# Kernel optimization log

Measured on AMD Instinct MI355X. Metric: run time of the kernel, lower is better.

The kernel has to match this reference:

```python
import jax, jax.numpy as jnp
import numpy as np

N = 100000   # nodes
E = 1600000  # edges
IN, HID, OUT = 128, 128, 64  # hidden = 2 * out_channels per GCNEncoder


def setup_inputs() -> dict:
    key = jax.random.key(0)
    k = jax.random.split(key, 5)
    x = jax.random.normal(k[0], (N, IN), dtype=jnp.float32)
    edge_index = jax.random.randint(k[1], (2, E), 0, N, dtype=jnp.int32)
    # Glorot-style init like PyG GCNConv
    W1 = jax.random.normal(k[2], (IN, HID), dtype=jnp.float32) * (1.0 / np.sqrt(IN))
    b1 = jnp.zeros((HID,), dtype=jnp.float32)
    W2 = jax.random.normal(k[3], (HID, OUT), dtype=jnp.float32) * (1.0 / np.sqrt(HID))
    b2 = jnp.zeros((OUT,), dtype=jnp.float32)
    return {"x": x, "edge_index": edge_index, "W1": W1, "b1": b1, "W2": W2, "b2": b2}


def gcn_conv(x, row, col, W, b):
    # x: [N, F_in]; row/col: [E+N] (edge_index with self-loops appended)
    h = x @ W                                      # dense transform [N, F_out]
    deg = jax.ops.segment_sum(jnp.ones_like(col, dtype=h.dtype), col, num_segments=N)
    dinv = jnp.where(deg > 0, jax.lax.rsqrt(deg), 0.0)
    norm = dinv[row] * dinv[col]                   # symmetric normalization per edge
    msg = h[row] * norm[:, None]                   # gather + scale: [E+N, F_out]
    out = jax.ops.segment_sum(msg, col, num_segments=N)  # scatter-add to targets
    return out + b


def reference(x, edge_index, W1, b1, W2, b2):
    loops = jnp.arange(N, dtype=edge_index.dtype)
    row = jnp.concatenate([edge_index[0], loops])  # sources
    col = jnp.concatenate([edge_index[1], loops])  # targets
    h = jax.nn.relu(gcn_conv(x, row, col, W1, b1))
    return gcn_conv(h, row, col, W2, b2)
```

## Files before the change

### kernel.cpp

```cpp
#include <hip/hip_runtime.h>
#include <hip/hip_fp16.h>

#define N_NODES 100000
#define N_EDGES 1600000
#define K_DIM   128

#define CHUNK_LG 8
#define CHUNK    256
#define NBKT     ((N_NODES + CHUNK - 1) / CHUNK)
#define CAP      4608
#define EPB      1024
#define NBLK_A   ((N_EDGES + EPB - 1) / EPB)
#define G1_BLOCKS ((N_NODES + 63) / 64)

typedef _Float16 half8 __attribute__((ext_vector_type(8)));
typedef float    f32x4 __attribute__((ext_vector_type(4)));

__global__ __launch_bounds__(256) void k_gemm1_bucket(
    const float* __restrict__ x, const float* __restrict__ W,
    _Float16* __restrict__ Hout,
    const int* __restrict__ row, const int* __restrict__ col,
    int* __restrict__ gcur, int* __restrict__ pairs)
{
    __shared__ __align__(16) char smem[128 * 136 * 2];

    if (blockIdx.x & 1) {
        constexpr int KD = K_DIM, NOUT = 128, NT = NOUT / 16;
        _Float16 (*Blds)[KD + 8] = reinterpret_cast<_Float16(*)[KD + 8]>(smem);

        for (int i = threadIdx.x * 4; i < KD * NOUT; i += 256 * 4) {
            int k = i / NOUT, n = i % NOUT;
            float4 wv = *reinterpret_cast<const float4*>(W + i);
            Blds[n + 0][k] = (_Float16)wv.x;
            Blds[n + 1][k] = (_Float16)wv.y;
            Blds[n + 2][k] = (_Float16)wv.z;
            Blds[n + 3][k] = (_Float16)wv.w;
        }
        __syncthreads();

        const int tile = blockIdx.x >> 1;
        const int wave = threadIdx.x >> 6;
        const int lane = threadIdx.x & 63;
        const int r16  = lane & 15;
        const int kg   = lane >> 4;
        const int arow = tile * 64 + wave * 16 + r16;
        const bool rowok = arow < N_NODES;

        f32x4 acc[NT];
#pragma unroll
        for (int ct = 0; ct < NT; ++ct) acc[ct] = (f32x4){0.f, 0.f, 0.f, 0.f};

#pragma unroll
        for (int kc = 0; kc < KD / 32; ++kc) {
            const int k0 = kc * 32 + kg * 8;
            float4 xa = make_float4(0.f, 0.f, 0.f, 0.f), xb = xa;
            if (rowok) {
                const float4* ap = reinterpret_cast<const float4*>(
                    x + (size_t)arow * KD + k0);
                xa = ap[0]; xb = ap[1];
            }
            half8 a;
            a[0] = (_Float16)xa.x; a[1] = (_Float16)xa.y;
            a[2] = (_Float16)xa.z; a[3] = (_Float16)xa.w;
            a[4] = (_Float16)xb.x; a[5] = (_Float16)xb.y;
            a[6] = (_Float16)xb.z; a[7] = (_Float16)xb.w;
#pragma unroll
            for (int ct = 0; ct < NT; ++ct) {
                half8 b = *reinterpret_cast<const half8*>(&Blds[ct * 16 + r16][k0]);
                acc[ct] = __builtin_amdgcn_mfma_f32_16x16x32_f16(a, b, acc[ct], 0, 0, 0);
            }
        }

        const int orow0 = tile * 64 + wave * 16 + kg * 4;
#pragma unroll
        for (int r = 0; r < 4; ++r) {
            int orow = orow0 + r;
            if (orow < N_NODES) {
#pragma unroll
                for (int ct = 0; ct < NT; ++ct)
                    Hout[(size_t)orow * NOUT + ct * 16 + r16] = (_Float16)acc[ct][r];
            }
        }
    } else {
        int* hist  = (int*)smem;
        int* sbase = hist + 512;
        int* lcur  = hist + 1024;
        int t = threadIdx.x;
        for (int i = t; i < NBKT; i += 256) { hist[i] = 0; lcur[i] = 0; }
        __syncthreads();
        int base = (blockIdx.x >> 1) * EPB;
        int myb[4], myp[4];
#pragma unroll
        for (int j = 0; j < 4; ++j) {
            int i = base + t + j * 256;
            int b = -1, p = 0;
            if (i < N_EDGES) {
                int r = row[i], c = col[i];
                b = c >> CHUNK_LG;
                p = ((c & (CHUNK - 1)) << 17) | r;
                atomicAdd(&hist[b], 1);
            }
            myb[j] = b; myp[j] = p;
        }
        __syncthreads();
        for (int i = t; i < NBKT; i += 256) {
            int c = hist[i];
            sbase[i] = c ? atomicAdd(&gcur[i], c) : 0;
        }
        __syncthreads();
#pragma unroll
        for (int j = 0; j < 4; ++j) {
            int b = myb[j];
            if (b >= 0) {
                int pos = sbase[b] + atomicAdd(&lcur[b], 1);
                pairs[b * CAP + pos] = myp[j];
            }
        }
    }
}

__global__ __launch_bounds__(256) void k_fillB(const int* __restrict__ gcur,
                                               const int* __restrict__ pairs,
                                               int* __restrict__ rowptr,
                                               float* __restrict__ dinv,
                                               int* __restrict__ srows) {
    __shared__ int red[256];
    __shared__ int psum[256];
    __shared__ int deg[CHUNK];
    __shared__ int curs[CHUNK];
    int b = blockIdx.x, t = threadIdx.x;

    int part = 0;
    for (int i = t; i < NBKT; i += 256)
        if (i < b) part += gcur[i];
    red[t] = part;
    __syncthreads();
    for (int off = 128; off; off >>= 1) {
        if (t < off) red[t] += red[t + off];
        __syncthreads();
    }
    int gb = red[0];
    int cnt = gcur[b];
    if (b == 0 && t == 0) rowptr[N_NODES] = N_EDGES;

    int nbase = b << CHUNK_LG;
    const int* mp = pairs + b * CAP;

    deg[t] = 0;
    __syncthreads();
    for (int i = t; i < cnt; i += 256) atomicAdd(&deg[mp[i] >> 17], 1);
    __syncthreads();

    int d = deg[t];
    psum[t] = d;
    __syncthreads();
    for (int off = 1; off < 256; off <<= 1) {
        int u = (t >= off) ? psum[t - off] : 0;
        __syncthreads();
        psum[t] += u;
        __syncthreads();
    }
    int o = gb + psum[t] - d;
    curs[t] = o;
    int node = nbase + t;
    if (node < N_NODES) {
        rowptr[node] = o;
        dinv[node] = rsqrtf(1.f + (float)d);
    }
    __syncthreads();
    for (int i = t; i < cnt; i += 256) {
        int v = mp[i];
        int pos = atomicAdd(&curs[v >> 17], 1);
        srows[pos] = v & 0x1FFFF;
    }
}

template<int NOUT>
__global__ __launch_bounds__(256) void k_gemm_mfma2(
    const _Float16* __restrict__ Ah, const float* __restrict__ W,
    const float* __restrict__ b_in, _Float16* __restrict__ Hout, int nrows)
{
    constexpr int KD = K_DIM;
    constexpr int NT = NOUT / 16;
    __shared__ _Float16 Blds[NOUT][KD + 8];

    for (int i = threadIdx.x * 4; i < KD * NOUT; i += 256 * 4) {
        int k = i / NOUT, n = i % NOUT;
        float4 wv = *reinterpret_cast<const float4*>(W + i);
        Blds[n + 0][k] = (_Float16)wv.x;
        Blds[n + 1][k] = (_Float16)wv.y;
        Blds[n + 2][k] = (_Float16)wv.z;
        Blds[n + 3][k] = (_Float16)wv.w;
    }
    __syncthreads();

    const int wave = threadIdx.x >> 6;
    const int lane = threadIdx.x & 63;
    const int r16  = lane & 15;
    const int kg   = lane >> 4;
    const int arow = blockIdx.x * 64 + wave * 16 + r16;
    const bool rowok = arow < nrows;

    f32x4 acc[NT];
#pragma unroll
    for (int ct = 0; ct < NT; ++ct) acc[ct] = (f32x4){0.f, 0.f, 0.f, 0.f};

#pragma unroll
    for (int kc = 0; kc < KD / 32; ++kc) {
        const int k0 = kc * 32 + kg * 8;
        uint4 raw = make_uint4(0, 0, 0, 0);
        if (rowok)
            raw = *reinterpret_cast<const uint4*>(Ah + (size_t)arow * KD + k0);
        union { uint4 u; _Float16 h[8]; } U; U.u = raw;
        float4 bA = *reinterpret_cast<const float4*>(b_in + k0);
        float4 bB = *reinterpret_cast<const float4*>(b_in + k0 + 4);
        half8 a;
        a[0] = (_Float16)fmaxf((float)U.h[0] + bA.x, 0.f);
        a[1] = (_Float16)fmaxf((float)U.h[1] + bA.y, 0.f);
        a[2] = (_Float16)fmaxf((float)U.h[2] + bA.z, 0.f);
        a[3] = (_Float16)fmaxf((float)U.h[3] + bA.w, 0.f);
        a[4] = (_Float16)fmaxf((float)U.h[4] + bB.x, 0.f);
        a[5] = (_Float16)fmaxf((float)U.h[5] + bB.y, 0.f);
        a[6] = (_Float16)fmaxf((float)U.h[6] + bB.z, 0.f);
        a[7] = (_Float16)fmaxf((float)U.h[7] + bB.w, 0.f);
#pragma unroll
        for (int ct = 0; ct < NT; ++ct) {
            half8 b = *reinterpret_cast<const half8*>(&Blds[ct * 16 + r16][k0]);
            acc[ct] = __builtin_amdgcn_mfma_f32_16x16x32_f16(a, b, acc[ct], 0, 0, 0);
        }
    }

    const int orow0 = blockIdx.x * 64 + wave * 16 + kg * 4;
#pragma unroll
    for (int r = 0; r < 4; ++r) {
        int orow = orow0 + r;
        if (orow < nrows) {
#pragma unroll
            for (int ct = 0; ct < NT; ++ct)
                Hout[(size_t)orow * NOUT + ct * 16 + r16] = (_Float16)acc[ct][r];
        }
    }
}

__device__ __forceinline__ void fma8(uint4 v, float wgt, float (&acc)[8]) {
    union { uint4 u; _Float16 h[8]; } U;
    U.u = v;
#pragma unroll
    for (int j = 0; j < 8; ++j)
        acc[j] = fmaf((float)U.h[j], wgt, acc[j]);
}

template<int F, bool OUT_HALF>
__global__ __launch_bounds__(256) void k_gather_h(
    const int* __restrict__ rowptr, const int* __restrict__ srows,
    const float* __restrict__ dinv, const _Float16* __restrict__ H,
    const float* __restrict__ bias, void* __restrict__ OUT, int n)
{
    constexpr int LPR = F / 8;
    constexpr int GR  = 64 / LPR;
    int w = blockIdx.x * 4 + (threadIdx.x >> 6);
    if (w >= n) return;
    int lane = threadIdx.x & 63;
    int g = lane / LPR;
    int c = lane % LPR;
    float di = dinv[w];
    int s = rowptr[w], e = rowptr[w + 1];
    const uint4* Hp = reinterpret_cast<const uint4*>(H);

    float acc[8];
#pragma unroll
    for (int j = 0; j < 8; ++j) acc[j] = 0.f;
    uint4 hv = Hp[(size_t)w * LPR + c];
    fma8(hv, (g == 0) ? di * di : 0.f, acc);

    if (s < e) {
        int k0 = s + g;
        int kc = min(k0, e - 1);
        int r  = srows[kc];
        float wcur = (k0 < e) ? dinv[r] * di : 0.f;
        uint4 hcur = Hp[(size_t)r * LPR + c];
        for (int k = s + GR; k < e; k += GR) {
            int k1  = k + g;
            int kc1 = min(k1, e - 1);
            int r1  = srows[kc1];
            float wnxt = (k1 < e) ? dinv[r1] * di : 0.f;
            uint4 hnxt = Hp[(size_t)r1 * LPR + c];
            fma8(hcur, wcur, acc);
            wcur = wnxt; hcur = hnxt;
        }
        fma8(hcur, wcur, acc);
    }

#pragma unroll
    for (int m = 32; m >= LPR; m >>= 1) {
#pragma unroll
        for (int j = 0; j < 8; ++j)
            acc[j] += __shfl_xor(acc[j], m, 64);
    }

    if (g == 0) {
        if constexpr (OUT_HALF) {
            union { uint4 u; __half2 h[4]; } P;
#pragma unroll
            for (int j = 0; j < 4; ++j)
                P.h[j] = __floats2half2_rn(acc[2 * j], acc[2 * j + 1]);
            reinterpret_cast<uint4*>(OUT)[(size_t)w * LPR + c] = P.u;
        } else {
            const float4* bp = reinterpret_cast<const float4*>(bias + c * 8);
            float4 b0 = bp[0], b1 = bp[1];
            float4 o0 = make_float4(acc[0] + b0.x, acc[1] + b0.y,
                                    acc[2] + b0.z, acc[3] + b0.w);
            float4 o1 = make_float4(acc[4] + b1.x, acc[5] + b1.y,
                                    acc[6] + b1.z, acc[7] + b1.w);
            float* op = (float*)OUT + (size_t)w * F + c * 8;
            *reinterpret_cast<float4*>(op)     = o0;
            *reinterpret_cast<float4*>(op + 4) = o1;
        }
    }
}


extern "C" void kernel_launch(void* const* d_in, const int* in_sizes, int n_in,
                              void* d_out, int out_size, void* d_ws, size_t ws_size,
                              hipStream_t stream) {
    const float* x  = (const float*)d_in[0];
    const int*   ei = (const int*)  d_in[1];
    const float* W1 = (const float*)d_in[2];
    const float* b1 = (const float*)d_in[3];
    const float* W2 = (const float*)d_in[4];
    const float* b2 = (const float*)d_in[5];
    float* out = (float*)d_out;

    const int* row = ei;
    const int* col = ei + N_EDGES;

    char* ws = (char*)d_ws;
    int*   gcur   = (int*)ws;
    int*   rowptr = gcur + 512;
    float* dinv   = (float*)(rowptr + ((N_NODES + 256) & ~255));
    int*   srows  = (int*)(dinv + ((N_NODES + 255) & ~255));
    _Float16* bufH   = (_Float16*)(srows + ((N_EDGES + 255) & ~255));
    _Float16* bufAgg = bufH + (size_t)N_NODES * 128;
    int*   pairs  = (int*)bufAgg;

    hipMemsetAsync(gcur, 0, NBKT * sizeof(int), stream);
    k_gemm1_bucket<<<G1_BLOCKS + NBLK_A, 256, 0, stream>>>(
        x, W1, bufH, row, col, gcur, pairs);

    k_fillB<<<NBKT, 256, 0, stream>>>(gcur, pairs, rowptr, dinv, srows);

    k_gather_h<128, true><<<(N_NODES + 3) / 4, 256, 0, stream>>>(
        rowptr, srows, dinv, bufH, nullptr, bufAgg, N_NODES);

    k_gemm_mfma2<64><<<(N_NODES + 63) / 64, 256, 0, stream>>>(
        bufAgg, W2, b1, bufH, N_NODES);

    k_gather_h<64, false><<<(N_NODES + 3) / 4, 256, 0, stream>>>(
        rowptr, srows, dinv, bufH, b2, out, N_NODES);
}
```

Baseline: 216.5 us.

## Fuse first-layer aggregation with second GEMM and rebalance bucket blocks

Replaces the separate layer-1 gather kernel and the second MFMA GEMM with one kernel. Each block aggregates 32 nodes into shared memory, applies bias and ReLU, and multiplies by W2 with MFMA, so the aggregated 128-wide fp16 matrix is never written to or read back from global memory. The edge-bucketing part now handles 4096 edges per block, with bucket blocks interleaved one in five among the GEMM blocks. The CSR fill kernel stages each bucket's pairs in shared memory so they are read from global memory once instead of twice. In exchange, every fused block converts W2 into shared memory again, and the fused kernel's occupancy and register pressure differ from the split kernels.

After: 204.9 us. 1.06x faster.

```diff
diff --git a/kernel.cpp b/kernel.cpp
--- a/kernel.cpp
+++ b/kernel.cpp
@@ -9,9 +9,10 @@
 #define CHUNK    256
 #define NBKT     ((N_NODES + CHUNK - 1) / CHUNK)
 #define CAP      4608
-#define EPB      1024
+#define EPB      4096
 #define NBLK_A   ((N_EDGES + EPB - 1) / EPB)
 #define G1_BLOCKS ((N_NODES + 63) / 64)
+#define NBLK_TOT (G1_BLOCKS + NBLK_A)
 
 typedef _Float16 half8 __attribute__((ext_vector_type(8)));
 typedef float    f32x4 __attribute__((ext_vector_type(4)));
@@ -24,7 +25,7 @@
 {
     __shared__ __align__(16) char smem[128 * 136 * 2];
 
-    if (blockIdx.x & 1) {
+    if (blockIdx.x % 5 != 0) {
         constexpr int KD = K_DIM, NOUT = 128, NT = NOUT / 16;
         _Float16 (*Blds)[KD + 8] = reinterpret_cast<_Float16(*)[KD + 8]>(smem);
 
@@ -38,7 +39,7 @@
         }
         __syncthreads();
 
-        const int tile = blockIdx.x >> 1;
+        const int tile = blockIdx.x - blockIdx.x / 5 - 1;
         const int wave = threadIdx.x >> 6;
         const int lane = threadIdx.x & 63;
         const int r16  = lane & 15;
@@ -88,10 +89,10 @@
         int t = threadIdx.x;
         for (int i = t; i < NBKT; i += 256) { hist[i] = 0; lcur[i] = 0; }
         __syncthreads();
-        int base = (blockIdx.x >> 1) * EPB;
-        int myb[4], myp[4];
-#pragma unroll
-        for (int j = 0; j < 4; ++j) {
+        int base = (blockIdx.x / 5) * EPB;
+        int myb[16], myp[16];
+#pragma unroll
+        for (int j = 0; j < 16; ++j) {
             int i = base + t + j * 256;
             int b = -1, p = 0;
             if (i < N_EDGES) {
@@ -109,7 +110,7 @@
         }
         __syncthreads();
 #pragma unroll
-        for (int j = 0; j < 4; ++j) {
+        for (int j = 0; j < 16; ++j) {
             int b = myb[j];
             if (b >= 0) {
                 int pos = sbase[b] + atomicAdd(&lcur[b], 1);
@@ -124,6 +125,7 @@
                                                int* __restrict__ rowptr,
                                                float* __restrict__ dinv,
                                                int* __restrict__ srows) {
+    __shared__ int mpl[CAP];
     __shared__ int red[256];
     __shared__ int psum[256];
     __shared__ int deg[CHUNK];
@@ -134,6 +136,7 @@
     for (int i = t; i < NBKT; i += 256)
         if (i < b) part += gcur[i];
     red[t] = part;
+    deg[t] = 0;
     __syncthreads();
     for (int off = 128; off; off >>= 1) {
         if (t < off) red[t] += red[t + off];
@@ -146,9 +149,11 @@
     int nbase = b << CHUNK_LG;
     const int* mp = pairs + b * CAP;
 
-    deg[t] = 0;
-    __syncthreads();
-    for (int i = t; i < cnt; i += 256) atomicAdd(&deg[mp[i] >> 17], 1);
+    for (int i = t; i < cnt; i += 256) {
+        int v = mp[i];
+        mpl[i] = v;
+        atomicAdd(&deg[v >> 17], 1);
+    }
     __syncthreads();
 
     int d = deg[t];
@@ -169,76 +174,9 @@
     }
     __syncthreads();
     for (int i = t; i < cnt; i += 256) {
-        int v = mp[i];
+        int v = mpl[i];
         int pos = atomicAdd(&curs[v >> 17], 1);
         srows[pos] = v & 0x1FFFF;
-    }
-}
-
-template<int NOUT>
-__global__ __launch_bounds__(256) void k_gemm_mfma2(
-    const _Float16* __restrict__ Ah, const float* __restrict__ W,
-    const float* __restrict__ b_in, _Float16* __restrict__ Hout, int nrows)
-{
-    constexpr int KD = K_DIM;
-    constexpr int NT = NOUT / 16;
-    __shared__ _Float16 Blds[NOUT][KD + 8];
-
-    for (int i = threadIdx.x * 4; i < KD * NOUT; i += 256 * 4) {
-        int k = i / NOUT, n = i % NOUT;
-        float4 wv = *reinterpret_cast<const float4*>(W + i);
-        Blds[n + 0][k] = (_Float16)wv.x;
-        Blds[n + 1][k] = (_Float16)wv.y;
-        Blds[n + 2][k] = (_Float16)wv.z;
-        Blds[n + 3][k] = (_Float16)wv.w;
-    }
-    __syncthreads();
-
-    const int wave = threadIdx.x >> 6;
-    const int lane = threadIdx.x & 63;
-    const int r16  = lane & 15;
-    const int kg   = lane >> 4;
-    const int arow = blockIdx.x * 64 + wave * 16 + r16;
-    const bool rowok = arow < nrows;
-
-    f32x4 acc[NT];
-#pragma unroll
-    for (int ct = 0; ct < NT; ++ct) acc[ct] = (f32x4){0.f, 0.f, 0.f, 0.f};
-
-#pragma unroll
-    for (int kc = 0; kc < KD / 32; ++kc) {
-        const int k0 = kc * 32 + kg * 8;
-        uint4 raw = make_uint4(0, 0, 0, 0);
-        if (rowok)
-            raw = *reinterpret_cast<const uint4*>(Ah + (size_t)arow * KD + k0);
-        union { uint4 u; _Float16 h[8]; } U; U.u = raw;
-        float4 bA = *reinterpret_cast<const float4*>(b_in + k0);
-        float4 bB = *reinterpret_cast<const float4*>(b_in + k0 + 4);
-        half8 a;
-        a[0] = (_Float16)fmaxf((float)U.h[0] + bA.x, 0.f);
-        a[1] = (_Float16)fmaxf((float)U.h[1] + bA.y, 0.f);
-        a[2] = (_Float16)fmaxf((float)U.h[2] + bA.z, 0.f);
-        a[3] = (_Float16)fmaxf((float)U.h[3] + bA.w, 0.f);
-        a[4] = (_Float16)fmaxf((float)U.h[4] + bB.x, 0.f);
-        a[5] = (_Float16)fmaxf((float)U.h[5] + bB.y, 0.f);
-        a[6] = (_Float16)fmaxf((float)U.h[6] + bB.z, 0.f);
-        a[7] = (_Float16)fmaxf((float)U.h[7] + bB.w, 0.f);
-#pragma unroll
-        for (int ct = 0; ct < NT; ++ct) {
-            half8 b = *reinterpret_cast<const half8*>(&Blds[ct * 16 + r16][k0]);
-            acc[ct] = __builtin_amdgcn_mfma_f32_16x16x32_f16(a, b, acc[ct], 0, 0, 0);
-        }
-    }
-
-    const int orow0 = blockIdx.x * 64 + wave * 16 + kg * 4;
-#pragma unroll
-    for (int r = 0; r < 4; ++r) {
-        int orow = orow0 + r;
-        if (orow < nrows) {
-#pragma unroll
-            for (int ct = 0; ct < NT; ++ct)
-                Hout[(size_t)orow * NOUT + ct * 16 + r16] = (_Float16)acc[ct][r];
-        }
     }
 }
 
@@ -248,6 +186,109 @@
 #pragma unroll
     for (int j = 0; j < 8; ++j)
         acc[j] = fmaf((float)U.h[j], wgt, acc[j]);
+}
+
+#define GG_NODES 32
+__global__ __launch_bounds__(512, 6) void k_gather_gemm2(
+    const int* __restrict__ rowptr, const int* __restrict__ srows,
+    const float* __restrict__ dinv, const _Float16* __restrict__ H,
+    const float* __restrict__ W2, const float* __restrict__ b1,
+    _Float16* __restrict__ H2, int n)
+{
+    __shared__ _Float16 Wlds[64][K_DIM + 8];
+    __shared__ _Float16 aggT[GG_NODES][K_DIM + 8];
+
+    for (int i = threadIdx.x * 4; i < K_DIM * 64; i += 512 * 4) {
+        int k = i >> 6, nn = i & 63;
+        float4 wv = *reinterpret_cast<const float4*>(W2 + i);
+        Wlds[nn + 0][k] = (_Float16)wv.x;
+        Wlds[nn + 1][k] = (_Float16)wv.y;
+        Wlds[nn + 2][k] = (_Float16)wv.z;
+        Wlds[nn + 3][k] = (_Float16)wv.w;
+    }
+
+    const int wid  = threadIdx.x >> 6;
+    const int lane = threadIdx.x & 63;
+    const int g = lane >> 4;
+    const int c = lane & 15;
+    const uint4* Hp = reinterpret_cast<const uint4*>(H);
+
+    for (int rr = 0; rr < 4; ++rr) {
+        int local = wid * 4 + rr;
+        int w = blockIdx.x * GG_NODES + local;
+        float acc[8];
+#pragma unroll
+        for (int j = 0; j < 8; ++j) acc[j] = 0.f;
+        if (w < n) {
+            float di = dinv[w];
+            int s = rowptr[w], e = rowptr[w + 1];
+            uint4 hv = Hp[(size_t)w * 16 + c];
+            fma8(hv, (g == 0) ? di * di : 0.f, acc);
+            if (s < e) {
+                int k0 = s + g;
+                int kc = min(k0, e - 1);
+                int r  = srows[kc];
+                float wcur = (k0 < e) ? dinv[r] * di : 0.f;
+                uint4 hcur = Hp[(size_t)r * 16 + c];
+                for (int k = s + 4; k < e; k += 4) {
+                    int k1  = k + g;
+                    int kc1 = min(k1, e - 1);
+                    int r1  = srows[kc1];
+                    float wnxt = (k1 < e) ? dinv[r1] * di : 0.f;
+                    uint4 hnxt = Hp[(size_t)r1 * 16 + c];
+                    fma8(hcur, wcur, acc);
+                    wcur = wnxt; hcur = hnxt;
+                }
+                fma8(hcur, wcur, acc);
+            }
+        }
+#pragma unroll
+        for (int m = 32; m >= 16; m >>= 1) {
+#pragma unroll
+            for (int j = 0; j < 8; ++j)
+                acc[j] += __shfl_xor(acc[j], m, 64);
+        }
+        if (g == 0) {
+            union { uint4 u; __half2 h[4]; } P;
+#pragma unroll
+            for (int j = 0; j < 4; ++j)
+                P.h[j] = __floats2half2_rn(acc[2 * j], acc[2 * j + 1]);
+            *reinterpret_cast<uint4*>(&aggT[local][c * 8]) = P.u;
+        }
+    }
+    __syncthreads();
+
+    const int r16 = lane & 15;
+    const int kg  = lane >> 4;
+    const int rtile = (wid & 1) * 16;
+    const int ctile = (wid >> 1) * 16;
+    f32x4 acc2 = (f32x4){0.f, 0.f, 0.f, 0.f};
+#pragma unroll
+    for (int kc = 0; kc < K_DIM / 32; ++kc) {
+        const int k0 = kc * 32 + kg * 8;
+        half8 raw = *reinterpret_cast<const half8*>(&aggT[rtile + r16][k0]);
+        float4 bA = *reinterpret_cast<const float4*>(b1 + k0);
+        float4 bB = *reinterpret_cast<const float4*>(b1 + k0 + 4);
+        half8 a;
+        a[0] = (_Float16)fmaxf((float)raw[0] + bA.x, 0.f);
+        a[1] = (_Float16)fmaxf((float)raw[1] + bA.y, 0.f);
+        a[2] = (_Float16)fmaxf((float)raw[2] + bA.z, 0.f);
+        a[3] = (_Float16)fmaxf((float)raw[3] + bA.w, 0.f);
+        a[4] = (_Float16)fmaxf((float)raw[4] + bB.x, 0.f);
+        a[5] = (_Float16)fmaxf((float)raw[5] + bB.y, 0.f);
+        a[6] = (_Float16)fmaxf((float)raw[6] + bB.z, 0.f);
+        a[7] = (_Float16)fmaxf((float)raw[7] + bB.w, 0.f);
+        half8 b = *reinterpret_cast<const half8*>(&Wlds[ctile + r16][k0]);
+        acc2 = __builtin_amdgcn_mfma_f32_16x16x32_f16(a, b, acc2, 0, 0, 0);
+    }
+    const int colg = ctile + r16;
+    const int row0 = blockIdx.x * GG_NODES + rtile + kg * 4;
+#pragma unroll
+    for (int r = 0; r < 4; ++r) {
+        int orow = row0 + r;
+        if (orow < n)
+            H2[(size_t)orow * 64 + colg] = (_Float16)acc2[r];
+    }
 }
 
 template<int F, bool OUT_HALF>
@@ -307,11 +348,11 @@
             reinterpret_cast<uint4*>(OUT)[(size_t)w * LPR + c] = P.u;
         } else {
             const float4* bp = reinterpret_cast<const float4*>(bias + c * 8);
-            float4 b0 = bp[0], b1 = bp[1];
+            float4 b0 = bp[0], b1v = bp[1];
             float4 o0 = make_float4(acc[0] + b0.x, acc[1] + b0.y,
                                     acc[2] + b0.z, acc[3] + b0.w);
-            float4 o1 = make_float4(acc[4] + b1.x, acc[5] + b1.y,
-                                    acc[6] + b1.z, acc[7] + b1.w);
+            float4 o1 = make_float4(acc[4] + b1v.x, acc[5] + b1v.y,
+                                    acc[6] + b1v.z, acc[7] + b1v.w);
             float* op = (float*)OUT + (size_t)w * F + c * 8;
             *reinterpret_cast<float4*>(op)     = o0;
             *reinterpret_cast<float4*>(op + 4) = o1;
@@ -339,22 +380,19 @@
     int*   rowptr = gcur + 512;
     float* dinv   = (float*)(rowptr + ((N_NODES + 256) & ~255));
     int*   srows  = (int*)(dinv + ((N_NODES + 255) & ~255));
-    _Float16* bufH   = (_Float16*)(srows + ((N_EDGES + 255) & ~255));
-    _Float16* bufAgg = bufH + (size_t)N_NODES * 128;
-    int*   pairs  = (int*)bufAgg;
+    _Float16* bufH  = (_Float16*)(srows + ((N_EDGES + 255) & ~255));
+    _Float16* bufH2 = bufH + (size_t)N_NODES * 128;
+    int*   pairs  = (int*)(bufH2 + (size_t)N_NODES * 64);
 
     hipMemsetAsync(gcur, 0, NBKT * sizeof(int), stream);
-    k_gemm1_bucket<<<G1_BLOCKS + NBLK_A, 256, 0, stream>>>(
+    k_gemm1_bucket<<<NBLK_TOT, 256, 0, stream>>>(
         x, W1, bufH, row, col, gcur, pairs);
 
     k_fillB<<<NBKT, 256, 0, stream>>>(gcur, pairs, rowptr, dinv, srows);
 
-    k_gather_h<128, true><<<(N_NODES + 3) / 4, 256, 0, stream>>>(
-        rowptr, srows, dinv, bufH, nullptr, bufAgg, N_NODES);
-
-    k_gemm_mfma2<64><<<(N_NODES + 63) / 64, 256, 0, stream>>>(
-        bufAgg, W2, b1, bufH, N_NODES);
+    k_gather_gemm2<<<(N_NODES + GG_NODES - 1) / GG_NODES, 512, 0, stream>>>(
+        rowptr, srows, dinv, bufH, W2, b1, bufH2, N_NODES);
 
     k_gather_h<64, false><<<(N_NODES + 3) / 4, 256, 0, stream>>>(
-        rowptr, srows, dinv, bufH, b2, out, N_NODES);
-}
+        rowptr, srows, dinv, bufH2, b2, out, N_NODES);
+}
```

## Pre-transpose weights to fp16, rebalance bucketing blocks, cache bucket pairs in LDS

Applied to the files above, without the earlier changes.

A small new kernel converts W1 and W2 to fp16 and transposes them once per call. Both GEMM kernels can then fill LDS with vectorized half8 copies instead of per-block float loads with scattered transposed LDS stores. The edge-bucketing part of the fused first kernel now handles 4096 edges per block, interleaved one bucketing block per four GEMM blocks, which cuts per-block histogram and global-atomic overhead but raises register use per thread. k_fillB stages its bucket's pairs in shared memory so it reads global memory once instead of twice. Layer 2 writes to a separate buffer so that pairs no longer alias the aggregation buffer.

Result: faster. 191.8 us (-11.4%).

```diff
diff --git a/kernel.cpp b/kernel.cpp
--- a/kernel.cpp
+++ b/kernel.cpp
@@ -9,36 +9,51 @@
 #define CHUNK    256
 #define NBKT     ((N_NODES + CHUNK - 1) / CHUNK)
 #define CAP      4608
-#define EPB      1024
+#define EPB      4096
 #define NBLK_A   ((N_EDGES + EPB - 1) / EPB)
 #define G1_BLOCKS ((N_NODES + 63) / 64)
+#define NBLK_TOT (G1_BLOCKS + NBLK_A)
 
 typedef _Float16 half8 __attribute__((ext_vector_type(8)));
 typedef float    f32x4 __attribute__((ext_vector_type(4)));
 
+__global__ __launch_bounds__(256) void k_prepW(const float* __restrict__ W1,
+                                               const float* __restrict__ W2,
+                                               _Float16* __restrict__ Wt1,
+                                               _Float16* __restrict__ Wt2) {
+    int c = blockIdx.x * 256 + threadIdx.x;
+    const float* W; _Float16* Wt; int nout;
+    if (c < 2048) { W = W1; Wt = Wt1; nout = 128; }
+    else          { W = W2; Wt = Wt2; nout = 64; c -= 2048; }
+    int n  = c >> 4;
+    int k0 = (c & 15) * 8;
+    half8 v;
+#pragma unroll
+    for (int j = 0; j < 8; ++j)
+        v[j] = (_Float16)W[(size_t)(k0 + j) * nout + n];
+    *reinterpret_cast<half8*>(Wt + (size_t)n * K_DIM + k0) = v;
+}
+
 __global__ __launch_bounds__(256) void k_gemm1_bucket(
-    const float* __restrict__ x, const float* __restrict__ W,
+    const float* __restrict__ x, const _Float16* __restrict__ Wt,
     _Float16* __restrict__ Hout,
     const int* __restrict__ row, const int* __restrict__ col,
     int* __restrict__ gcur, int* __restrict__ pairs)
 {
     __shared__ __align__(16) char smem[128 * 136 * 2];
 
-    if (blockIdx.x & 1) {
+    if (blockIdx.x % 5 != 0) {
         constexpr int KD = K_DIM, NOUT = 128, NT = NOUT / 16;
         _Float16 (*Blds)[KD + 8] = reinterpret_cast<_Float16(*)[KD + 8]>(smem);
 
-        for (int i = threadIdx.x * 4; i < KD * NOUT; i += 256 * 4) {
-            int k = i / NOUT, n = i % NOUT;
-            float4 wv = *reinterpret_cast<const float4*>(W + i);
-            Blds[n + 0][k] = (_Float16)wv.x;
-            Blds[n + 1][k] = (_Float16)wv.y;
-            Blds[n + 2][k] = (_Float16)wv.z;
-            Blds[n + 3][k] = (_Float16)wv.w;
-        }
-        __syncthreads();
-
-        const int tile = blockIdx.x >> 1;
+        for (int i = threadIdx.x; i < NOUT * (KD / 8); i += 256) {
+            int n = i >> 4, k0 = (i & 15) * 8;
+            *reinterpret_cast<half8*>(&Blds[n][k0]) =
+                *reinterpret_cast<const half8*>(Wt + (size_t)n * KD + k0);
+        }
+        __syncthreads();
+
+        const int tile = blockIdx.x - blockIdx.x / 5 - 1;
         const int wave = threadIdx.x >> 6;
         const int lane = threadIdx.x & 63;
         const int r16  = lane & 15;
@@ -88,10 +103,10 @@
         int t = threadIdx.x;
         for (int i = t; i < NBKT; i += 256) { hist[i] = 0; lcur[i] = 0; }
         __syncthreads();
-        int base = (blockIdx.x >> 1) * EPB;
-        int myb[4], myp[4];
-#pragma unroll
-        for (int j = 0; j < 4; ++j) {
+        int base = (blockIdx.x / 5) * EPB;
+        int myb[16], myp[16];
+#pragma unroll
+        for (int j = 0; j < 16; ++j) {
             int i = base + t + j * 256;
             int b = -1, p = 0;
             if (i < N_EDGES) {
@@ -109,7 +124,7 @@
         }
         __syncthreads();
 #pragma unroll
-        for (int j = 0; j < 4; ++j) {
+        for (int j = 0; j < 16; ++j) {
             int b = myb[j];
             if (b >= 0) {
                 int pos = sbase[b] + atomicAdd(&lcur[b], 1);
@@ -124,6 +139,7 @@
                                                int* __restrict__ rowptr,
                                                float* __restrict__ dinv,
                                                int* __restrict__ srows) {
+    __shared__ int mpl[CAP];
     __shared__ int red[256];
     __shared__ int psum[256];
     __shared__ int deg[CHUNK];
@@ -134,6 +150,7 @@
     for (int i = t; i < NBKT; i += 256)
         if (i < b) part += gcur[i];
     red[t] = part;
+    deg[t] = 0;
     __syncthreads();
     for (int off = 128; off; off >>= 1) {
         if (t < off) red[t] += red[t + off];
@@ -146,9 +163,11 @@
     int nbase = b << CHUNK_LG;
     const int* mp = pairs + b * CAP;
 
-    deg[t] = 0;
-    __syncthreads();
-    for (int i = t; i < cnt; i += 256) atomicAdd(&deg[mp[i] >> 17], 1);
+    for (int i = t; i < cnt; i += 256) {
+        int v = mp[i];
+        mpl[i] = v;
+        atomicAdd(&deg[v >> 17], 1);
+    }
     __syncthreads();
 
     int d = deg[t];
@@ -169,7 +188,7 @@
     }
     __syncthreads();
     for (int i = t; i < cnt; i += 256) {
-        int v = mp[i];
+        int v = mpl[i];
         int pos = atomicAdd(&curs[v >> 17], 1);
         srows[pos] = v & 0x1FFFF;
     }
@@ -177,20 +196,17 @@
 
 template<int NOUT>
 __global__ __launch_bounds__(256) void k_gemm_mfma2(
-    const _Float16* __restrict__ Ah, const float* __restrict__ W,
+    const _Float16* __restrict__ Ah, const _Float16* __restrict__ Wt,
     const float* __restrict__ b_in, _Float16* __restrict__ Hout, int nrows)
 {
     constexpr int KD = K_DIM;
     constexpr int NT = NOUT / 16;
     __shared__ _Float16 Blds[NOUT][KD + 8];
 
-    for (int i = threadIdx.x * 4; i < KD * NOUT; i += 256 * 4) {
-        int k = i / NOUT, n = i % NOUT;
-        float4 wv = *reinterpret_cast<const float4*>(W + i);
-        Blds[n + 0][k] = (_Float16)wv.x;
-        Blds[n + 1][k] = (_Float16)wv.y;
-        Blds[n + 2][k] = (_Float16)wv.z;
-        Blds[n + 3][k] = (_Float16)wv.w;
+    for (int i = threadIdx.x; i < NOUT * (KD / 8); i += 256) {
+        int n = i >> 4, k0 = (i & 15) * 8;
+        *reinterpret_cast<half8*>(&Blds[n][k0]) =
+            *reinterpret_cast<const half8*>(Wt + (size_t)n * KD + k0);
     }
     __syncthreads();
 
@@ -307,11 +323,11 @@
             reinterpret_cast<uint4*>(OUT)[(size_t)w * LPR + c] = P.u;
         } else {
             const float4* bp = reinterpret_cast<const float4*>(bias + c * 8);
-            float4 b0 = bp[0], b1 = bp[1];
+            float4 b0 = bp[0], b1v = bp[1];
             float4 o0 = make_float4(acc[0] + b0.x, acc[1] + b0.y,
                                     acc[2] + b0.z, acc[3] + b0.w);
-            float4 o1 = make_float4(acc[4] + b1.x, acc[5] + b1.y,
-                                    acc[6] + b1.z, acc[7] + b1.w);
+            float4 o1 = make_float4(acc[4] + b1v.x, acc[5] + b1v.y,
+                                    acc[6] + b1v.z, acc[7] + b1v.w);
             float* op = (float*)OUT + (size_t)w * F + c * 8;
             *reinterpret_cast<float4*>(op)     = o0;
             *reinterpret_cast<float4*>(op + 4) = o1;
@@ -339,13 +355,18 @@
     int*   rowptr = gcur + 512;
     float* dinv   = (float*)(rowptr + ((N_NODES + 256) & ~255));
     int*   srows  = (int*)(dinv + ((N_NODES + 255) & ~255));
-    _Float16* bufH   = (_Float16*)(srows + ((N_EDGES + 255) & ~255));
+    _Float16* bufH  = (_Float16*)(srows + ((N_EDGES + 255) & ~255));
     _Float16* bufAgg = bufH + (size_t)N_NODES * 128;
-    int*   pairs  = (int*)bufAgg;
+    _Float16* bufH2  = bufAgg + (size_t)N_NODES * 128;
+    _Float16* Wt1 = bufH2 + (size_t)N_NODES * 64;
+    _Float16* Wt2 = Wt1 + 128 * 128;
+    int*   pairs  = (int*)(Wt2 + 64 * 128 + 256);
 
     hipMemsetAsync(gcur, 0, NBKT * sizeof(int), stream);
-    k_gemm1_bucket<<<G1_BLOCKS + NBLK_A, 256, 0, stream>>>(
-        x, W1, bufH, row, col, gcur, pairs);
+    k_prepW<<<12, 256, 0, stream>>>(W1, W2, Wt1, Wt2);
+
+    k_gemm1_bucket<<<NBLK_TOT, 256, 0, stream>>>(
+        x, Wt1, bufH, row, col, gcur, pairs);
 
     k_fillB<<<NBKT, 256, 0, stream>>>(gcur, pairs, rowptr, dinv, srows);
 
@@ -353,8 +374,8 @@
         rowptr, srows, dinv, bufH, nullptr, bufAgg, N_NODES);
 
     k_gemm_mfma2<64><<<(N_NODES + 63) / 64, 256, 0, stream>>>(
-        bufAgg, W2, b1, bufH, N_NODES);
+        bufAgg, Wt2, b1, bufH2, N_NODES);
 
     k_gather_h<64, false><<<(N_NODES + 3) / 4, 256, 0, stream>>>(
-        rowptr, srows, dinv, bufH, b2, out, N_NODES);
-}
+        rowptr, srows, dinv, bufH2, b2, out, N_NODES);
+}
```
